# Optimization experiments

Measured on AMD Instinct MI355X. Metric: run time of the kernel, lower is better.

Reference implementation:

```python
import jax, jax.numpy as jnp
import numpy as np
import math

B, T, D, DI, DFF, H = 4, 1024, 1024, 256, 4096, 16
S, N, E = 16, 256, 1024          # stat_num, token_num, exemplar_len
STAT_K, TOKEN_K = 8, 16
NEG = -1e6


def setup_inputs() -> dict:
    key = jax.random.key(0)
    ks = jax.random.split(key, 32)
    r = lambda i, shape: jax.random.normal(ks[i], shape, jnp.float32)
    w = lambda i, shape: r(i, shape) * 0.02
    return dict(
        x=r(0, (B, T, D)),
        stat_enc=r(1, (B * S, N, D)),
        exemplar_enc=r(2, (B, E, D)),
        stat_feature=r(3, (B, S, D)),
        intent_embed=r(4, (B, 1, DI)),
        Wq1=w(5, (D, D)), Wk1=w(6, (D, D)), Wv1=w(7, (D, D)), Wo1=w(8, (D, D)),
        Wq_stat=w(9, (D + DI, D)), Wq_token=w(10, (D + DI, D)),
        Wk_stat=w(11, (D, D)), Wk_token=w(12, (D, D)),
        Wv_sel=w(13, (D, D)), Wo_sel=w(14, (D, D)),
        Wq2=w(15, (D + DI, D)), Wk2=w(16, (D, D)), Wv2=w(17, (D, D)), Wo2=w(18, (D, D)),
        Wg=w(19, (2 * D, 1)),
        W1=w(20, (D, DFF)), b1=jnp.zeros((DFF,), jnp.float32),
        W2=w(21, (DFF, D)), b2=jnp.zeros((D,), jnp.float32),
        g1=jnp.ones((D,), jnp.float32), be1=jnp.zeros((D,), jnp.float32),
        g2=jnp.ones((D,), jnp.float32), be2=jnp.zeros((D,), jnp.float32),
        g3=jnp.ones((D,), jnp.float32), be3=jnp.zeros((D,), jnp.float32),
        stat_valid_len=jax.random.randint(ks[22], (B,), 1, S + 1),
        example_valid_len=jax.random.randint(ks[23], (B,), 1, E + 1),
    )


def _ln(x, g, b):
    m = x.mean(-1, keepdims=True)
    v = ((x - m) ** 2).mean(-1, keepdims=True)
    return (x - m) / jnp.sqrt(v + 1e-5) * g + b


def _mha(q, k, v, valid, Wq, Wk, Wv, Wo):
    Bq, Tq, _ = q.shape
    Sk = k.shape[1]
    sp = lambda z: z.reshape(Bq, z.shape[1], H, -1).transpose(0, 2, 1, 3)  # B,H,L,dh
    qh, kh, vh = sp(q @ Wq), sp(k @ Wk), sp(v @ Wv)
    dh = qh.shape[-1]
    sc = jnp.einsum('bhtd,bhsd->bhts', qh, kh) / math.sqrt(dh)
    vl = valid[:, None, None, None] if valid.ndim == 1 else valid[:, None, :, None]
    sc = jnp.where(jnp.arange(Sk)[None, None, None, :] < vl, sc, NEG)
    w = jax.nn.softmax(sc, axis=-1)
    out = jnp.einsum('bhts,bhsd->bhtd', w, vh).transpose(0, 2, 1, 3).reshape(Bq, Tq, -1)
    return out @ Wo


def _scatter_topk(scores, k):
    # keep top-k per row, everything else -> NEG (matches torch topk+scatter)
    shp = scores.shape
    flat = scores.reshape(-1, shp[-1])
    vals, idx = jax.lax.top_k(flat, k)
    out = jnp.full_like(flat, NEG).at[jnp.arange(flat.shape[0])[:, None], idx].set(vals)
    return out.reshape(shp)


def reference(x, stat_enc, exemplar_enc, stat_feature, intent_embed,
              Wq1, Wk1, Wv1, Wo1,
              Wq_stat, Wq_token, Wk_stat, Wk_token, Wv_sel, Wo_sel,
              Wq2, Wk2, Wv2, Wo2, Wg,
              W1, b1, W2, b2,
              g1, be1, g2, be2, g3, be3,
              stat_valid_len, example_valid_len):
    # masked self-attention (training mode -> causal valid lens)
    dec_valid = jnp.broadcast_to(jnp.arange(1, T + 1)[None, :], (B, T))
    x2 = _mha(x, x, x, dec_valid, Wq1, Wk1, Wv1, Wo1)
    y = _ln(x + x2, g1, be1)
    yi = jnp.concatenate([y, jnp.broadcast_to(intent_embed, (B, T, DI))], axis=-1)

    # selective hierarchical top-k attention
    qs = yi @ Wq_stat                      # [B,T,D]
    qt = yi @ Wq_token                     # [B,T,D]
    ks = stat_feature @ Wk_stat            # [B,S,D]
    kt = (stat_enc @ Wk_token).reshape(B, S, N, D)
    vv = (stat_enc @ Wv_sel).reshape(B, S, N, D)
    scale = math.sqrt(D)
    ssc = jnp.einsum('btd,bsd->bts', qs, ks) / scale
    ssc = jnp.where(jnp.arange(S)[None, None, :] < stat_valid_len[:, None, None], ssc, NEG)
    sw = jax.nn.softmax(_scatter_topk(ssc, min(S - 1, STAT_K)), axis=-1)   # [B,T,S]
    tsc = jnp.einsum('btd,bsnd->btsn', qt, kt) / scale                      # [B,T,S,N]
    tw = jax.nn.softmax(_scatter_topk(tsc, min(N - 1, TOKEN_K)), axis=-1)
    comb = sw[..., None] * tw                                               # [B,T,S,N]
    y2s = jnp.einsum('btsn,bsnd->btd', comb, vv) @ Wo_sel

    # exemplar cross-attention
    y2e = _mha(yi, exemplar_enc, exemplar_enc, example_valid_len, Wq2, Wk2, Wv2, Wo2)

    gate = jax.nn.sigmoid(jnp.concatenate([y2s, y2e], axis=-1) @ Wg)
    y2 = gate * y2s + (1.0 - gate) * y2e
    z = _ln(y + 2.0 * y2, g2, be2)
    ffn = jax.nn.relu(z @ W1 + b1) @ W2 + b2
    return _ln(z + ffn, g3, be3)
```

## Files before the change

### kernel.cpp

```cpp
#include <hip/hip_runtime.h>

typedef unsigned short u16;
typedef short s16x8 __attribute__((ext_vector_type(8)));
typedef u16 u16x4 __attribute__((ext_vector_type(4)));
typedef float f32x4 __attribute__((ext_vector_type(4)));

#define T_N   1024
#define NEGV  -1e6f
#define MB    (1L << 20)

__device__ __forceinline__ u16 f2bf(float f) {
    unsigned u = __float_as_uint(f);
    u += 0x7fffu + ((u >> 16) & 1u);
    return (u16)(u >> 16);
}
__device__ __forceinline__ float bf2f(u16 h) {
    return __uint_as_float(((unsigned)h) << 16);
}
__device__ __forceinline__ f32x4 mfma16(s16x8 a, s16x8 b, f32x4 c) {
    return __builtin_amdgcn_mfma_f32_16x16x32_bf16(a, b, c, 0, 0, 0);
}
__device__ __forceinline__ void gll16(const u16* g, u16* l) {
    __builtin_amdgcn_global_load_lds((const __attribute__((address_space(1))) void*)g,
                                     (__attribute__((address_space(3))) void*)l, 16, 0, 0);
}

struct P6 { const float* s[6]; u16* d[6]; };

__global__ __launch_bounds__(256) void transpose_cast_batch(P6 pp, int K, int N) {
    const float* __restrict__ src = pp.s[blockIdx.z];
    u16* __restrict__ dst = pp.d[blockIdx.z];
    __shared__ float tile[32][33];
    int nb = blockIdx.x * 32, kb = blockIdx.y * 32;
    int tx = threadIdx.x & 31, ty = threadIdx.x >> 5;
    #pragma unroll
    for (int i = 0; i < 4; i++)
        tile[ty + 8*i][tx] = src[(long)(kb + ty + 8*i) * N + nb + tx];
    __syncthreads();
    #pragma unroll
    for (int i = 0; i < 4; i++)
        dst[(long)(nb + ty + 8*i) * K + kb + tx] = f2bf(tile[tx][ty + 8*i]);
}

__global__ __launch_bounds__(256) void cast_bf16_kernel(const float* __restrict__ src,
                                                        u16* __restrict__ dst, long n) {
    long i = ((long)blockIdx.x * 256 + threadIdx.x) * 4;
    if (i >= n) return;
    float4 v = *(const float4*)(src + i);
    u16x4 o = { f2bf(v.x), f2bf(v.y), f2bf(v.z), f2bf(v.w) };
    *(u16x4*)(dst + i) = o;
}

template<typename OutT, bool RELU, bool HAS_BIAS>
__global__ __launch_bounds__(256) void gemm_bt(
    const u16* __restrict__ A, const u16* __restrict__ Bt, OutT* __restrict__ C,
    const float* __restrict__ bias, int M, int N, int K,
    int lda, int ldb, int ldc,
    int batchDivA, long sA, long sB, long sC)
{
    A  += (long)(blockIdx.z / batchDivA) * sA;
    Bt += (long)blockIdx.z * sB;
    C  += (long)blockIdx.z * sC;
    __shared__ __align__(16) u16 As[4096];
    __shared__ __align__(16) u16 Bs[4096];
    const int tid = threadIdx.x;
    const int wave = tid >> 6, lane = tid & 63;
    const int quad = lane >> 4, l16 = lane & 15;
    const int wr = (wave >> 1) * 64, wc = (wave & 1) * 64;
    const long row0 = (long)blockIdx.y * 128, col0 = (long)blockIdx.x * 128;

    f32x4 acc[4][4] = {};

    const int l4r = lane >> 2;
    const int l4c = (lane & 3) * 8;
    const int ra = wave * 32 + l4r;
    const u16* Ap0 = A + (row0 + ra) * (long)lda + l4c;
    const u16* Ap1 = Ap0 + 16L * lda;
    const u16* Bp0 = Bt + (col0 + ra) * (long)ldb + l4c;
    const u16* Bp1 = Bp0 + 16L * ldb;
    u16* AsW0 = &As[(wave * 32) * 32];
    u16* AsW1 = &As[(wave * 32 + 16) * 32];
    u16* BsW0 = &Bs[(wave * 32) * 32];
    u16* BsW1 = &Bs[(wave * 32 + 16) * 32];
    const bool aok0 = (row0 + wave * 32) < M;
    const bool aok1 = (row0 + wave * 32 + 16) < M;

    for (int k0 = 0; k0 < K; k0 += 32) {
        __syncthreads();
        if (aok0) gll16(Ap0 + k0, AsW0);
        if (aok1) gll16(Ap1 + k0, AsW1);
        gll16(Bp0 + k0, BsW0);
        gll16(Bp1 + k0, BsW1);
        __syncthreads();
        s16x8 af[4], bfr[4];
        #pragma unroll
        for (int i = 0; i < 4; i++)
            af[i]  = *(const s16x8*)&As[(wr + i*16 + l16) * 32 + quad*8];
        #pragma unroll
        for (int j = 0; j < 4; j++)
            bfr[j] = *(const s16x8*)&Bs[(wc + j*16 + l16) * 32 + quad*8];
        #pragma unroll
        for (int i = 0; i < 4; i++)
            #pragma unroll
            for (int j = 0; j < 4; j++)
                acc[i][j] = mfma16(af[i], bfr[j], acc[i][j]);
    }

    #pragma unroll
    for (int i = 0; i < 4; i++) {
        long row = row0 + wr + i*16 + quad*4;
        #pragma unroll
        for (int j = 0; j < 4; j++) {
            long col = col0 + wc + j*16 + l16;
            float bv = 0.f;
            if constexpr (HAS_BIAS) bv = bias[col];
            #pragma unroll
            for (int r = 0; r < 4; r++) {
                if (row + r < M) {
                    float v = acc[i][j][r] + bv;
                    if constexpr (RELU) v = fmaxf(v, 0.f);
                    if constexpr (sizeof(OutT) == 2) C[(row + r) * (long)ldc + col] = f2bf(v);
                    else                             C[(row + r) * (long)ldc + col] = v;
                }
            }
        }
    }
}

template<typename OutT, bool RELU, bool HAS_BIAS>
__global__ __launch_bounds__(512, 2) void gemm_bt256(
    const u16* __restrict__ A, const u16* __restrict__ Bt, OutT* __restrict__ C,
    const float* __restrict__ bias, int M, int N, int K,
    int lda, int ldb, int ldc,
    int batchDivA, long sA, long sB, long sC)
{
    int bx = blockIdx.x, by = blockIdx.y;
    {
        const int nwg = gridDim.x * gridDim.y;
        if ((nwg & 7) == 0) {
            const int flat = by * gridDim.x + bx;
            const int nf = (flat & 7) * (nwg >> 3) + (flat >> 3);
            bx = nf % gridDim.x;
            by = nf / gridDim.x;
        }
    }
    A  += (long)(blockIdx.z / batchDivA) * sA;
    Bt += (long)blockIdx.z * sB;
    C  += (long)blockIdx.z * sC;
    __shared__ __align__(16) u16 As[4][8192];
    __shared__ __align__(16) u16 Bs[4][8192];
    const int tid = threadIdx.x;
    const int wave = tid >> 6, lane = tid & 63;
    const int quad = lane >> 4, l16 = lane & 15;
    const int wm = wave >> 2, wn = wave & 3;
    const long row0 = (long)by * 256, col0 = (long)bx * 256;

    const int srow = tid >> 2;
    const int scol = ((tid & 3) ^ ((srow >> 1) & 3)) * 8;
    const u16* Ag = A  + (row0 + srow) * (long)lda + scol;
    const u16* Bg = Bt + (col0 + srow) * (long)ldb + scol;
    const int ldsoff = wave * 512;

    f32x4 acc[8][4] = {};
    const int NT = K >> 5;

    auto stageA = [&](int kt, int buf) {
        gll16(Ag + (long)kt * 32,            &As[buf][ldsoff]);
        gll16(Ag + (long)kt * 32 + 128L*lda, &As[buf][4096 + ldsoff]);
    };
    auto stageB = [&](int kt, int buf) {
        gll16(Bg + (long)kt * 32,            &Bs[buf][ldsoff]);
        gll16(Bg + (long)kt * 32 + 128L*ldb, &Bs[buf][4096 + ldsoff]);
    };

    stageA(0, 0); stageB(0, 0);
    stageA(1, 1); stageB(1, 1);
    stageA(2, 2); stageB(2, 2);
    asm volatile("s_waitcnt vmcnt(8)" ::: "memory");
    __builtin_amdgcn_s_barrier();
    __builtin_amdgcn_sched_barrier(0);

    const int arow = wm * 128 + l16;
    const int brow = wn * 64  + l16;
    const int kq   = (quad ^ ((l16 >> 1) & 3)) * 8;

    for (int kt = 0; kt < NT; ++kt) {
        const int b  = kt & 3;
        const int sb = (kt + 3) & 3;
        const bool st = (kt + 3) < NT;
        const u16* Ab = As[b];
        const u16* Bb = Bs[b];

        s16x8 bfr[4], af[8];
        #pragma unroll
        for (int j = 0; j < 4; ++j)
            bfr[j] = *(const s16x8*)&Bb[(brow + j*16) * 32 + kq];
        #pragma unroll
        for (int i = 0; i < 8; ++i)
            af[i] = *(const s16x8*)&Ab[(arow + i*16) * 32 + kq];

        if (st) { stageA(kt + 3, sb); stageB(kt + 3, sb); }

        #pragma unroll
        for (int i = 0; i < 8; ++i)
            #pragma unroll
            for (int j = 0; j < 4; ++j)
                acc[i][j] = mfma16(af[i], bfr[j], acc[i][j]);

        const int rem = NT - 2 - kt;
        if (rem >= 2)      asm volatile("s_waitcnt vmcnt(8)" ::: "memory");
        else if (rem == 1) asm volatile("s_waitcnt vmcnt(4)" ::: "memory");
        else if (rem == 0) asm volatile("s_waitcnt vmcnt(0)" ::: "memory");
        __builtin_amdgcn_s_barrier();
        __builtin_amdgcn_sched_barrier(0);
    }

    #pragma unroll
    for (int i = 0; i < 8; ++i) {
        const long row = row0 + wm*128 + i*16 + quad*4;
        #pragma unroll
        for (int j = 0; j < 4; ++j) {
            const long col = col0 + wn*64 + j*16 + l16;
            float bv = 0.f;
            if constexpr (HAS_BIAS) bv = bias[col];
            #pragma unroll
            for (int r = 0; r < 4; ++r) {
                float v = acc[i][j][r] + bv;
                if constexpr (RELU) v = fmaxf(v, 0.f);
                if constexpr (sizeof(OutT) == 2) C[(row + r) * (long)ldc + col] = f2bf(v);
                else                             C[(row + r) * (long)ldc + col] = v;
            }
        }
    }
}

template<bool CAUSAL>
__global__ __launch_bounds__(256) void flash_attn_kernel(
    const u16* __restrict__ Q, const u16* __restrict__ Kg, const u16* __restrict__ Vg,
    const int* __restrict__ valid_len, u16* __restrict__ O,
    int qld, int kld, int vld)
{
    const int h = blockIdx.y, b = blockIdx.z;
    const int qt0 = blockIdx.x * 64;
    const int tid = threadIdx.x;
    const int wave = tid >> 6, lane = tid & 63;
    const int quad = lane >> 4, l16 = lane & 15;

    __shared__ __align__(16) u16 Qs[64][72];
    __shared__ __align__(16) u16 Ks[64][72];
    __shared__ __align__(16) u16 Vt[64][72];
    __shared__ __align__(16) u16 Ps[4][16][72];

    const int sr = tid >> 2, scc = (tid & 3) * 16;
    {
        const u16* qp = Q + ((long)b * T_N + qt0 + sr) * qld + h * 64 + scc;
        *(s16x8*)&Qs[sr][scc]     = *(const s16x8*)qp;
        *(s16x8*)&Qs[sr][scc + 8] = *(const s16x8*)(qp + 8);
    }
    float m_i[4] = {-1e30f, -1e30f, -1e30f, -1e30f};
    float l_i[4] = {0.f, 0.f, 0.f, 0.f};
    f32x4 o_acc[4] = {};

    int vl = 0, kend;
    if (CAUSAL) kend = qt0 + 64;
    else { vl = valid_len[b]; kend = (vl + 63) & ~63; }

    for (int kv0 = 0; kv0 < kend; kv0 += 64) {
        __syncthreads();
        {
            const u16* kp = Kg + ((long)b * T_N + kv0 + sr) * kld + h * 64 + scc;
            *(s16x8*)&Ks[sr][scc]     = *(const s16x8*)kp;
            *(s16x8*)&Ks[sr][scc + 8] = *(const s16x8*)(kp + 8);
            const u16* vp = Vg + ((long)b * T_N + kv0 + sr) * vld + h * 64 + scc;
            s16x8 v0 = *(const s16x8*)vp;
            s16x8 v1 = *(const s16x8*)(vp + 8);
            #pragma unroll
            for (int j = 0; j < 8; j++) {
                Vt[scc + j][sr]     = (u16)v0[j];
                Vt[scc + 8 + j][sr] = (u16)v1[j];
            }
        }
        __syncthreads();
        f32x4 sc[4] = {};
        #pragma unroll
        for (int kk = 0; kk < 64; kk += 32) {
            s16x8 aq = *(const s16x8*)&Qs[wave*16 + l16][kk + quad*8];
            #pragma unroll
            for (int j = 0; j < 4; j++) {
                s16x8 bk = *(const s16x8*)&Ks[j*16 + l16][kk + quad*8];
                sc[j] = mfma16(aq, bk, sc[j]);
            }
        }
        const int qrow = qt0 + wave*16 + quad*4;
        #pragma unroll
        for (int j = 0; j < 4; j++) {
            int kcol = kv0 + j*16 + l16;
            #pragma unroll
            for (int r = 0; r < 4; r++) {
                float s = sc[j][r] * 0.125f;
                bool ok = CAUSAL ? (kcol <= qrow + r) : (kcol < vl);
                sc[j][r] = ok ? s : -1e30f;
            }
        }
        float alpha[4];
        #pragma unroll
        for (int r = 0; r < 4; r++) {
            float mx = fmaxf(fmaxf(sc[0][r], sc[1][r]), fmaxf(sc[2][r], sc[3][r]));
            #pragma unroll
            for (int d = 1; d < 16; d <<= 1) mx = fmaxf(mx, __shfl_xor(mx, d, 64));
            float mn = fmaxf(m_i[r], mx);
            alpha[r] = __expf(m_i[r] - mn);
            m_i[r] = mn;
        }
        float rsum[4] = {0.f, 0.f, 0.f, 0.f};
        #pragma unroll
        for (int j = 0; j < 4; j++)
            #pragma unroll
            for (int r = 0; r < 4; r++) {
                float pv = __expf(sc[j][r] - m_i[r]);
                sc[j][r] = pv;
                rsum[r] += pv;
            }
        #pragma unroll
        for (int r = 0; r < 4; r++) {
            #pragma unroll
            for (int d = 1; d < 16; d <<= 1) rsum[r] += __shfl_xor(rsum[r], d, 64);
            l_i[r] = l_i[r] * alpha[r] + rsum[r];
        }
        #pragma unroll
        for (int j = 0; j < 4; j++)
            #pragma unroll
            for (int r = 0; r < 4; r++)
                Ps[wave][quad*4 + r][j*16 + l16] = f2bf(sc[j][r]);
        #pragma unroll
        for (int j2 = 0; j2 < 4; j2++)
            #pragma unroll
            for (int r = 0; r < 4; r++)
                o_acc[j2][r] *= alpha[r];
        __syncthreads();
        #pragma unroll
        for (int kk = 0; kk < 64; kk += 32) {
            s16x8 ap = *(const s16x8*)&Ps[wave][l16][kk + quad*8];
            #pragma unroll
            for (int j2 = 0; j2 < 4; j2++) {
                s16x8 bv = *(const s16x8*)&Vt[j2*16 + l16][kk + quad*8];
                o_acc[j2] = mfma16(ap, bv, o_acc[j2]);
            }
        }
    }
    #pragma unroll
    for (int j2 = 0; j2 < 4; j2++) {
        #pragma unroll
        for (int r = 0; r < 4; r++) {
            float v = o_acc[j2][r] / l_i[r];
            long row = (long)b * T_N + qt0 + wave*16 + quad*4 + r;
            O[row * 1024 + h*64 + j2*16 + l16] = f2bf(v);
        }
    }
}

__global__ __launch_bounds__(256) void ssc_kernel(
    const u16* __restrict__ qs, const u16* __restrict__ ks,
    const int* __restrict__ svl, float* __restrict__ ssc, int qld)
{
    const int t = blockIdx.x, b = blockIdx.y;
    const int wave = threadIdx.x >> 6, lane = threadIdx.x & 63;
    const u16* qrow = qs + ((long)b * T_N + t) * qld + lane * 16;
    const int vl = svl[b];
    for (int s = wave; s < 16; s += 4) {
        const u16* krow = ks + ((long)b * 16 + s) * 1024 + lane * 16;
        float acc = 0.f;
        #pragma unroll
        for (int seg = 0; seg < 2; seg++) {
            s16x8 qv = *(const s16x8*)(qrow + seg*8);
            s16x8 kv = *(const s16x8*)(krow + seg*8);
            #pragma unroll
            for (int j = 0; j < 8; j++) acc += bf2f((u16)qv[j]) * bf2f((u16)kv[j]);
        }
        #pragma unroll
        for (int d = 1; d < 64; d <<= 1) acc += __shfl_xor(acc, d, 64);
        if (lane == 0)
            ssc[((long)b * T_N + t) * 16 + s] = (s < vl) ? acc * (1.f/32.f) : NEGV;
    }
}

__global__ __launch_bounds__(256) void select_combine_kernel(
    const float* __restrict__ ssc, const float* __restrict__ tsc,
    const u16* __restrict__ vv, u16* __restrict__ out, int t0, int vld)
{
    const int tl = blockIdx.x, b = blockIdx.y;
    const int tg = t0 + tl;
    const int tid = threadIdx.x;
    const int wave = tid >> 6, lane = tid & 63;
    __shared__ float coeff[128];
    __shared__ long  rowoff[128];
    __shared__ int   sel_s[8];
    __shared__ float sel_w[8];

    if (wave == 0) {
        float cur = (lane < 16) ? ssc[((long)b * T_N + tg) * 16 + lane] : -3e38f;
        float mx0 = 0.f, ssum = 0.f, myv = -3e38f;
        int myi = 0;
        #pragma unroll
        for (int it = 0; it < 8; it++) {
            float mv = cur; int mi = lane;
            #pragma unroll
            for (int d = 1; d < 64; d <<= 1) {
                float ov = __shfl_xor(mv, d, 64);
                int   oi = __shfl_xor(mi, d, 64);
                if (ov > mv || (ov == mv && oi < mi)) { mv = ov; mi = oi; }
            }
            if (it == 0) mx0 = mv;
            ssum += __expf(mv - mx0);
            if (lane == it) { myv = mv; myi = mi; }
            if (lane == mi) cur = -3e38f;
        }
        if (lane < 8) { sel_s[lane] = myi; sel_w[lane] = __expf(myv - mx0) / ssum; }
    }
    __syncthreads();

    for (int slot = wave; slot < 8; slot += 4) {
        int s = sel_s[slot];
        float sw = sel_w[slot];
        const float* trow = tsc + (((long)b * 16 + s) * 512 + tl) * 256;
        float4 lv4 = *(const float4*)(trow + lane * 4);
        float loc[4] = { lv4.x, lv4.y, lv4.z, lv4.w };
        float mx0 = 0.f, tsum = 0.f, myv = -3e38f;
        int myi = 0;
        for (int it = 0; it < 16; it++) {
            float mv = -3e38f; int mi = 0;
            #pragma unroll
            for (int u = 0; u < 4; u++)
                if (loc[u] > mv) { mv = loc[u]; mi = lane*4 + u; }
            #pragma unroll
            for (int d = 1; d < 64; d <<= 1) {
                float ov = __shfl_xor(mv, d, 64);
                int   oi = __shfl_xor(mi, d, 64);
                if (ov > mv || (ov == mv && oi < mi)) { mv = ov; mi = oi; }
            }
            if (it == 0) mx0 = mv * (1.f/32.f);
            tsum += __expf(mv * (1.f/32.f) - mx0);
            if (lane == it) { myv = mv; myi = mi; }
            if ((mi >> 2) == lane) {
                int u = mi & 3;
                if (u == 0) loc[0] = -3e38f;
                else if (u == 1) loc[1] = -3e38f;
                else if (u == 2) loc[2] = -3e38f;
                else loc[3] = -3e38f;
            }
        }
        if (lane < 16) {
            coeff[slot * 16 + lane]  = sw * __expf(myv * (1.f/32.f) - mx0) / tsum;
            rowoff[slot * 16 + lane] = (long)((b * 16 + s) * 256 + myi) * vld;
        }
    }
    __syncthreads();

    const int d0 = tid * 4;
    float a0 = 0.f, a1 = 0.f, a2 = 0.f, a3 = 0.f;
    for (int r = 0; r < 128; r++) {
        float c = coeff[r];
        const u16* vp = vv + rowoff[r] + d0;
        u16x4 v4 = *(const u16x4*)vp;
        a0 += c * bf2f(v4[0]);
        a1 += c * bf2f(v4[1]);
        a2 += c * bf2f(v4[2]);
        a3 += c * bf2f(v4[3]);
    }
    u16x4 o4 = { f2bf(a0), f2bf(a1), f2bf(a2), f2bf(a3) };
    *(u16x4*)(out + ((long)b * T_N + tg) * 1024 + d0) = o4;
}

__device__ __forceinline__ float block_sum(float v, float* red) {
    #pragma unroll
    for (int d = 1; d < 64; d <<= 1) v += __shfl_xor(v, d, 64);
    __syncthreads();
    if ((threadIdx.x & 63) == 0) red[threadIdx.x >> 6] = v;
    __syncthreads();
    return red[0] + red[1] + red[2] + red[3];
}

__global__ __launch_bounds__(256) void ln1_kernel(
    const float* __restrict__ x, const float* __restrict__ x2,
    const float* __restrict__ intent, const float* __restrict__ g, const float* __restrict__ be,
    u16* __restrict__ yi)
{
    __shared__ float red[4];
    const long row = blockIdx.x;
    const int tid = threadIdx.x;
    const long base = row * 1024 + tid * 4;
    float4 xv = *(const float4*)(x + base);
    float4 dv = *(const float4*)(x2 + base);
    float h0 = xv.x + dv.x, h1 = xv.y + dv.y, h2 = xv.z + dv.z, h3 = xv.w + dv.w;
    float s1 = block_sum(h0 + h1 + h2 + h3, red);
    float s2 = block_sum(h0*h0 + h1*h1 + h2*h2 + h3*h3, red);
    float mean = s1 * (1.f/1024.f);
    float var = s2 * (1.f/1024.f) - mean * mean;
    float inv = rsqrtf(var + 1e-5f);
    const int c = tid * 4;
    float4 gv = *(const float4*)(g + c);
    float4 bv = *(const float4*)(be + c);
    float o0 = (h0 - mean) * inv * gv.x + bv.x;
    float o1 = (h1 - mean) * inv * gv.y + bv.y;
    float o2 = (h2 - mean) * inv * gv.z + bv.z;
    float o3 = (h3 - mean) * inv * gv.w + bv.w;
    u16x4 ob = { f2bf(o0), f2bf(o1), f2bf(o2), f2bf(o3) };
    *(u16x4*)(yi + row * 1280 + c) = ob;
    const int b = (int)(row >> 10);
    yi[row * 1280 + 1024 + tid] = f2bf(intent[b * 256 + tid]);
}

__global__ __launch_bounds__(256) void gate_ln2_kernel(
    const u16* __restrict__ yi, const float* __restrict__ y2s, const float* __restrict__ y2e,
    const float* __restrict__ Wg, const float* __restrict__ g, const float* __restrict__ be,
    float* __restrict__ z, u16* __restrict__ zbf)
{
    __shared__ float red[4];
    const long row = blockIdx.x;
    const int tid = threadIdx.x;
    const long base = row * 1024 + tid * 4;
    const int c = tid * 4;
    float4 sv = *(const float4*)(y2s + base);
    float4 ev = *(const float4*)(y2e + base);
    float4 w1 = *(const float4*)(Wg + c);
    float4 w2 = *(const float4*)(Wg + 1024 + c);
    float dot = sv.x*w1.x + sv.y*w1.y + sv.z*w1.z + sv.w*w1.w
              + ev.x*w2.x + ev.y*w2.y + ev.z*w2.z + ev.w*w2.w;
    float tot = block_sum(dot, red);
    float gate = 1.f / (1.f + __expf(-tot));
    u16x4 yv4 = *(const u16x4*)(yi + row * 1280 + c);
    float h0 = bf2f(yv4[0]) + 2.f * (gate * sv.x + (1.f - gate) * ev.x);
    float h1 = bf2f(yv4[1]) + 2.f * (gate * sv.y + (1.f - gate) * ev.y);
    float h2 = bf2f(yv4[2]) + 2.f * (gate * sv.z + (1.f - gate) * ev.z);
    float h3 = bf2f(yv4[3]) + 2.f * (gate * sv.w + (1.f - gate) * ev.w);
    float s1 = block_sum(h0 + h1 + h2 + h3, red);
    float s2 = block_sum(h0*h0 + h1*h1 + h2*h2 + h3*h3, red);
    float mean = s1 * (1.f/1024.f);
    float var = s2 * (1.f/1024.f) - mean * mean;
    float inv = rsqrtf(var + 1e-5f);
    float4 gv = *(const float4*)(g + c);
    float4 bv = *(const float4*)(be + c);
    float o0 = (h0 - mean) * inv * gv.x + bv.x;
    float o1 = (h1 - mean) * inv * gv.y + bv.y;
    float o2 = (h2 - mean) * inv * gv.z + bv.z;
    float o3 = (h3 - mean) * inv * gv.w + bv.w;
    *(float4*)(z + base) = make_float4(o0, o1, o2, o3);
    u16x4 ob = { f2bf(o0), f2bf(o1), f2bf(o2), f2bf(o3) };
    *(u16x4*)(zbf + row * 1024 + c) = ob;
}

__global__ __launch_bounds__(256) void ln3_kernel(
    const float* __restrict__ z, const float* __restrict__ p0, const float* __restrict__ p1,
    const float* __restrict__ b2,
    const float* __restrict__ g, const float* __restrict__ be, float* __restrict__ out)
{
    __shared__ float red[4];
    const long row = blockIdx.x;
    const int tid = threadIdx.x;
    const long base = row * 1024 + tid * 4;
    const int c = tid * 4;
    float4 zv = *(const float4*)(z + base);
    float4 f0 = *(const float4*)(p0 + base);
    float4 f1 = *(const float4*)(p1 + base);
    float4 bb = *(const float4*)(b2 + c);
    float h0 = zv.x + f0.x + f1.x + bb.x;
    float h1 = zv.y + f0.y + f1.y + bb.y;
    float h2 = zv.z + f0.z + f1.z + bb.z;
    float h3 = zv.w + f0.w + f1.w + bb.w;
    float s1 = block_sum(h0 + h1 + h2 + h3, red);
    float s2 = block_sum(h0*h0 + h1*h1 + h2*h2 + h3*h3, red);
    float mean = s1 * (1.f/1024.f);
    float var = s2 * (1.f/1024.f) - mean * mean;
    float inv = rsqrtf(var + 1e-5f);
    float4 gv = *(const float4*)(g + c);
    float4 bv = *(const float4*)(be + c);
    float o0 = (h0 - mean) * inv * gv.x + bv.x;
    float o1 = (h1 - mean) * inv * gv.y + bv.y;
    float o2 = (h2 - mean) * inv * gv.z + bv.z;
    float o3 = (h3 - mean) * inv * gv.w + bv.w;
    *(float4*)(out + base) = make_float4(o0, o1, o2, o3);
}

extern "C" void kernel_launch(void* const* d_in, const int* in_sizes, int n_in,
                              void* d_out, int out_size, void* d_ws, size_t ws_size,
                              hipStream_t stream)
{
    (void)in_sizes; (void)n_in; (void)out_size; (void)ws_size;
    const float* x      = (const float*)d_in[0];
    const float* stat_e = (const float*)d_in[1];
    const float* exem   = (const float*)d_in[2];
    const float* sfeat  = (const float*)d_in[3];
    const float* intent = (const float*)d_in[4];
    const float* Wg  = (const float*)d_in[19];
    const float* b1  = (const float*)d_in[21];
    const float* b2  = (const float*)d_in[23];
    const float* g1  = (const float*)d_in[24]; const float* be1 = (const float*)d_in[25];
    const float* g2  = (const float*)d_in[26]; const float* be2 = (const float*)d_in[27];
    const float* g3  = (const float*)d_in[28]; const float* be3 = (const float*)d_in[29];
    const int* svl = (const int*)d_in[30];
    const int* evl = (const int*)d_in[31];
    float* outp = (float*)d_out;

    char* base = (char*)d_ws;
    u16*  bufA  = (u16*)(base + 0*MB);
    u16*  qkv1  = (u16*)(base + 8*MB);
    float* x2a  = (float*)(base + 8*MB);
    u16*  kv2   = (u16*)(base + 8*MB);
    u16*  w1t   = (u16*)(base + 8*MB);
    u16*  w2t   = (u16*)(base + 16*MB);
    u16*  yibf  = (u16*)(base + 32*MB);
    u16*  buf3  = (u16*)(base + 42*MB);
    u16*  zbf   = (u16*)(base + 42*MB);
    u16*  sebf  = (u16*)(base + 66*MB);
    float* tsch = (float*)(base + 66*MB);
    u16*  hid   = (u16*)(base + 66*MB);
    u16*  ktvv  = (u16*)(base + 98*MB);
    float* y2sf = (float*)(base + 98*MB);
    float* p0f  = (float*)(base + 98*MB);
    u16*  exbf  = (u16*)(base + 114*MB);
    float* y2ef = (float*)(base + 122*MB);
    float* zf   = (float*)(base + 138*MB);
    u16*  sfbf  = (u16*)(base + 162*MB);
    u16*  ksbf  = (u16*)(base + 162*MB + 256*1024);
    float* sscf = (float*)(base + 162*MB + 512*1024);
    char* wpool = base + 163*MB;

    dim3 blk(256);
    dim3 blk512(512);
    auto cast = [&](const float* s, u16* d, long n) {
        cast_bf16_kernel<<<dim3((unsigned)((n/4 + 255) / 256)), blk, 0, stream>>>(s, d, n);
    };
    auto g_n = [&](const u16* A, const u16* Bt, u16* C, int M, int N, int K,
                   int lda, int ldb, int ldc) {
        gemm_bt<u16,false,false><<<dim3(N/128, (M+127)/128, 1), blk, 0, stream>>>(
            A, Bt, C, nullptr, M, N, K, lda, ldb, ldc, 1, 0, 0, 0);
    };
    auto g_f = [&](const u16* A, const u16* Bt, float* C, int M, int N, int K,
                   int lda, int ldb, int ldc) {
        gemm_bt<float,false,false><<<dim3(N/128, (M+127)/128, 1), blk, 0, stream>>>(
            A, Bt, C, nullptr, M, N, K, lda, ldb, ldc, 1, 0, 0, 0);
    };
    auto g256_n = [&](const u16* A, const u16* Bt, u16* C, int M, int N, int K,
                      int lda, int ldb, int ldc) {
        gemm_bt256<u16,false,false><<<dim3(N/256, M/256, 1), blk512, 0, stream>>>(
            A, Bt, C, nullptr, M, N, K, lda, ldb, ldc, 1, 0, 0, 0);
    };

    u16* wqkv1t = (u16*)wpool;
    u16* wo1t   = (u16*)(wpool) + 3L*1024*1024;
    {
        P6 pp{};
        pp.s[0]=(const float*)d_in[5]; pp.d[0]=wqkv1t;
        pp.s[1]=(const float*)d_in[6]; pp.d[1]=wqkv1t + 1L*1024*1024;
        pp.s[2]=(const float*)d_in[7]; pp.d[2]=wqkv1t + 2L*1024*1024;
        pp.s[3]=(const float*)d_in[8]; pp.d[3]=wo1t;
        transpose_cast_batch<<<dim3(32, 32, 4), blk, 0, stream>>>(pp, 1024, 1024);
    }
    cast(x, bufA, 4096L*1024);
    g256_n(bufA, wqkv1t, qkv1, 4096, 3072, 1024, 1024, 1024, 3072);
    flash_attn_kernel<true><<<dim3(16, 16, 4), blk, 0, stream>>>(
        qkv1, qkv1 + 1024, qkv1 + 2048, nullptr, bufA, 3072, 3072, 3072);
    g_f(bufA, wo1t, x2a, 4096, 1024, 1024, 1024, 1024, 1024);
    ln1_kernel<<<dim3(4096), blk, 0, stream>>>(x, x2a, intent, g1, be1, yibf);

    u16* wq3t = (u16*)wpool;
    {
        P6 pp{};
        pp.s[0]=(const float*)d_in[9];  pp.d[0]=wq3t;
        pp.s[1]=(const float*)d_in[10]; pp.d[1]=wq3t + 1L*1024*1280;
        pp.s[2]=(const float*)d_in[15]; pp.d[2]=wq3t + 2L*1024*1280;
        transpose_cast_batch<<<dim3(32, 40, 3), blk, 0, stream>>>(pp, 1280, 1024);
    }
    g256_n(yibf, wq3t, buf3, 4096, 3072, 1280, 1280, 1280, 3072);
    u16* wkst = (u16*)wpool;
    u16* wkv  = (u16*)(wpool) + 1L*1024*1024;
    {
        P6 pp{};
        pp.s[0]=(const float*)d_in[11]; pp.d[0]=wkst;
        pp.s[1]=(const float*)d_in[12]; pp.d[1]=wkv;
        pp.s[2]=(const float*)d_in[13]; pp.d[2]=wkv + 1L*1024*1024;
        transpose_cast_batch<<<dim3(32, 32, 3), blk, 0, stream>>>(pp, 1024, 1024);
    }
    cast(sfeat, sfbf, 64L*1024);
    cast(stat_e, sebf, 16384L*1024);
    g_n(sfbf, wkst, ksbf, 64, 1024, 1024, 1024, 1024, 1024);
    g256_n(sebf, wkv, ktvv, 16384, 2048, 1024, 1024, 1024, 2048);
    ssc_kernel<<<dim3(1024, 4), blk, 0, stream>>>(buf3, ksbf, svl, sscf, 3072);
    for (int hh = 0; hh < 2; hh++) {
        long t0 = hh * 512;
        gemm_bt<float,false,false><<<dim3(2, 4, 64), blk, 0, stream>>>(
            buf3 + 1024 + t0*3072, ktvv, tsch, nullptr, 512, 256, 1024,
            3072, 2048, 256, 16, (long)T_N*3072, 256L*2048, 512L*256);
        select_combine_kernel<<<dim3(512, 4), blk, 0, stream>>>(
            sscf, tsch, ktvv + 1024, bufA, (int)t0, 2048);
    }
    u16* wost = (u16*)wpool;
    u16* wkv2 = (u16*)(wpool) + 1L*1024*1024;
    u16* wo2t = (u16*)(wpool) + 3L*1024*1024;
    {
        P6 pp{};
        pp.s[0]=(const float*)d_in[14]; pp.d[0]=wost;
        pp.s[1]=(const float*)d_in[16]; pp.d[1]=wkv2;
        pp.s[2]=(const float*)d_in[17]; pp.d[2]=wkv2 + 1L*1024*1024;
        pp.s[3]=(const float*)d_in[18]; pp.d[3]=wo2t;
        transpose_cast_batch<<<dim3(32, 32, 4), blk, 0, stream>>>(pp, 1024, 1024);
    }
    g_f(bufA, wost, y2sf, 4096, 1024, 1024, 1024, 1024, 1024);

    cast(exem, exbf, 4096L*1024);
    g_n(exbf, wkv2, kv2, 4096, 2048, 1024, 1024, 1024, 2048);
    flash_attn_kernel<false><<<dim3(16, 16, 4), blk, 0, stream>>>(
        buf3 + 2048, kv2, kv2 + 1024, evl, bufA, 3072, 2048, 2048);
    g_f(bufA, wo2t, y2ef, 4096, 1024, 1024, 1024, 1024, 1024);

    gate_ln2_kernel<<<dim3(4096), blk, 0, stream>>>(yibf, y2sf, y2ef, Wg, g2, be2, zf, zbf);

    {
        P6 pp{}; pp.s[0] = (const float*)d_in[20]; pp.d[0] = w1t;
        transpose_cast_batch<<<dim3(128, 32, 1), blk, 0, stream>>>(pp, 1024, 4096);
    }
    {
        P6 pp{}; pp.s[0] = (const float*)d_in[22]; pp.d[0] = w2t;
        transpose_cast_batch<<<dim3(32, 128, 1), blk, 0, stream>>>(pp, 4096, 1024);
    }
    gemm_bt256<u16,true,true><<<dim3(16, 16, 1), blk512, 0, stream>>>(
        zbf, w1t, hid, b1, 4096, 4096, 1024, 1024, 1024, 4096, 1, 0, 0, 0);
    gemm_bt<float,false,false><<<dim3(8, 32, 2), blk, 0, stream>>>(
        hid, w2t, p0f, nullptr, 4096, 1024, 2048, 4096, 4096, 1024,
        1, 2048, 2048, 4096L*1024);

    ln3_kernel<<<dim3(4096), blk, 0, stream>>>(zf, p0f, p0f + 4096L*1024, b2, g3, be3, outp);
}
```

Measured before the change: 1.005 ms.

## Double-buffer K/V tiles with register prefetch and swizzled LDS in flash attention

Restructures the flash attention loop so the next K/V tile is loaded from global memory into registers while the current tile is being computed, then stored into a second LDS buffer. This cuts the per-iteration barriers from two to one. Q fragments are held in registers rather than LDS, LDS arrays are unpadded with an XOR swizzle to avoid bank conflicts, and MFMA sections get raised wave priority. The kernel also gets an occupancy hint of 4 blocks per CU. Register pressure increases and the swizzled indexing adds address arithmetic.

```diff
diff --git a/kernel.cpp b/kernel.cpp
--- a/kernel.cpp
+++ b/kernel.cpp
@@ -23,6 +23,12 @@
 __device__ __forceinline__ void gll16(const u16* g, u16* l) {
     __builtin_amdgcn_global_load_lds((const __attribute__((address_space(1))) void*)g,
                                      (__attribute__((address_space(3))) void*)l, 16, 0, 0);
+}
+__device__ __forceinline__ int swzf(int row) {
+    return ((row >> 1) & 3) | ((row & 1) << 2);
+}
+__device__ __forceinline__ int swzc(int col, int row) {
+    return (((col >> 3) ^ swzf(row)) << 3) | (col & 7);
 }
 
 struct P6 { const float* s[6]; u16* d[6]; };
@@ -235,7 +241,7 @@
 }
 
 template<bool CAUSAL>
-__global__ __launch_bounds__(256) void flash_attn_kernel(
+__global__ __launch_bounds__(256, 4) void flash_attn_kernel(
     const u16* __restrict__ Q, const u16* __restrict__ Kg, const u16* __restrict__ Vg,
     const int* __restrict__ valid_len, u16* __restrict__ O,
     int qld, int kld, int vld)
@@ -246,17 +252,30 @@
     const int wave = tid >> 6, lane = tid & 63;
     const int quad = lane >> 4, l16 = lane & 15;
 
-    __shared__ __align__(16) u16 Qs[64][72];
-    __shared__ __align__(16) u16 Ks[64][72];
-    __shared__ __align__(16) u16 Vt[64][72];
-    __shared__ __align__(16) u16 Ps[4][16][72];
-
-    const int sr = tid >> 2, scc = (tid & 3) * 16;
-    {
-        const u16* qp = Q + ((long)b * T_N + qt0 + sr) * qld + h * 64 + scc;
-        *(s16x8*)&Qs[sr][scc]     = *(const s16x8*)qp;
-        *(s16x8*)&Qs[sr][scc + 8] = *(const s16x8*)(qp + 8);
-    }
+    __shared__ __align__(16) u16 Ks[2][64][64];
+    __shared__ __align__(16) u16 Vt[2][64][64];
+    __shared__ __align__(16) u16 Ps[4][16][64];
+
+    s16x8 aq[2];
+    {
+        const u16* qp = Q + ((long)b * T_N + qt0 + wave*16 + l16) * qld + h * 64 + quad * 8;
+        aq[0] = *(const s16x8*)qp;
+        aq[1] = *(const s16x8*)(qp + 32);
+    }
+
+    const int ksr = tid >> 2;
+    const int ks2 = (tid & 3) * 2;
+    const int vsr = tid & 63;
+    const int vd0 = (tid >> 6) * 16;
+
+    const u16* kp = Kg + ((long)b * T_N + ksr) * (long)kld + h * 64 + ks2 * 8;
+    const u16* vp = Vg + ((long)b * T_N + vsr) * (long)vld + h * 64 + vd0;
+    const long kstep = 64L * kld, vstep = 64L * vld;
+
+    const int fl  = swzf(l16);
+    const int kc0 = ((quad ^ fl) & 7) * 8;
+    const int kc1 = (((quad + 4) ^ fl) & 7) * 8;
+
     float m_i[4] = {-1e30f, -1e30f, -1e30f, -1e30f};
     float l_i[4] = {0.f, 0.f, 0.f, 0.f};
     f32x4 o_acc[4] = {};
@@ -264,39 +283,51 @@
     int vl = 0, kend;
     if (CAUSAL) kend = qt0 + 64;
     else { vl = valid_len[b]; kend = (vl + 63) & ~63; }
-
-    for (int kv0 = 0; kv0 < kend; kv0 += 64) {
-        __syncthreads();
-        {
-            const u16* kp = Kg + ((long)b * T_N + kv0 + sr) * kld + h * 64 + scc;
-            *(s16x8*)&Ks[sr][scc]     = *(const s16x8*)kp;
-            *(s16x8*)&Ks[sr][scc + 8] = *(const s16x8*)(kp + 8);
-            const u16* vp = Vg + ((long)b * T_N + kv0 + sr) * vld + h * 64 + scc;
-            s16x8 v0 = *(const s16x8*)vp;
-            s16x8 v1 = *(const s16x8*)(vp + 8);
-            #pragma unroll
-            for (int j = 0; j < 8; j++) {
-                Vt[scc + j][sr]     = (u16)v0[j];
-                Vt[scc + 8 + j][sr] = (u16)v1[j];
-            }
-        }
-        __syncthreads();
+    const int nt = kend >> 6;
+
+    s16x8 krA, krB, vrA, vrB;
+    krA = *(const s16x8*)kp;       krB = *(const s16x8*)(kp + 8);
+    vrA = *(const s16x8*)vp;       vrB = *(const s16x8*)(vp + 8);
+    kp += kstep; vp += vstep;
+    {
+        *(s16x8*)&Ks[0][ksr][swzc(ks2*8,     ksr)] = krA;
+        *(s16x8*)&Ks[0][ksr][swzc(ks2*8 + 8, ksr)] = krB;
+        #pragma unroll
+        for (int j = 0; j < 8; ++j) {
+            Vt[0][vd0 + j    ][swzc(vsr, vd0 + j    )] = (u16)vrA[j];
+            Vt[0][vd0 + 8 + j][swzc(vsr, vd0 + 8 + j)] = (u16)vrB[j];
+        }
+    }
+    __syncthreads();
+
+    for (int t = 0; t < nt; ++t) {
+        const int cur = t & 1;
+        const bool more = (t + 1) < nt;
+        if (more) {
+            krA = *(const s16x8*)kp;  krB = *(const s16x8*)(kp + 8);
+            vrA = *(const s16x8*)vp;  vrB = *(const s16x8*)(vp + 8);
+            kp += kstep; vp += vstep;
+        }
         f32x4 sc[4] = {};
-        #pragma unroll
-        for (int kk = 0; kk < 64; kk += 32) {
-            s16x8 aq = *(const s16x8*)&Qs[wave*16 + l16][kk + quad*8];
-            #pragma unroll
-            for (int j = 0; j < 4; j++) {
-                s16x8 bk = *(const s16x8*)&Ks[j*16 + l16][kk + quad*8];
-                sc[j] = mfma16(aq, bk, sc[j]);
-            }
-        }
+        __builtin_amdgcn_s_setprio(1);
+        #pragma unroll
+        for (int j = 0; j < 4; ++j) {
+            s16x8 bk0 = *(const s16x8*)&Ks[cur][j*16 + l16][kc0];
+            sc[j] = mfma16(aq[0], bk0, sc[j]);
+        }
+        #pragma unroll
+        for (int j = 0; j < 4; ++j) {
+            s16x8 bk1 = *(const s16x8*)&Ks[cur][j*16 + l16][kc1];
+            sc[j] = mfma16(aq[1], bk1, sc[j]);
+        }
+        __builtin_amdgcn_s_setprio(0);
+        const int kv0 = t * 64;
         const int qrow = qt0 + wave*16 + quad*4;
         #pragma unroll
-        for (int j = 0; j < 4; j++) {
+        for (int j = 0; j < 4; ++j) {
             int kcol = kv0 + j*16 + l16;
             #pragma unroll
-            for (int r = 0; r < 4; r++) {
+            for (int r = 0; r < 4; ++r) {
                 float s = sc[j][r] * 0.125f;
                 bool ok = CAUSAL ? (kcol <= qrow + r) : (kcol < vl);
                 sc[j][r] = ok ? s : -1e30f;
@@ -304,7 +335,7 @@
         }
         float alpha[4];
         #pragma unroll
-        for (int r = 0; r < 4; r++) {
+        for (int r = 0; r < 4; ++r) {
             float mx = fmaxf(fmaxf(sc[0][r], sc[1][r]), fmaxf(sc[2][r], sc[3][r]));
             #pragma unroll
             for (int d = 1; d < 16; d <<= 1) mx = fmaxf(mx, __shfl_xor(mx, d, 64));
@@ -314,44 +345,62 @@
         }
         float rsum[4] = {0.f, 0.f, 0.f, 0.f};
         #pragma unroll
-        for (int j = 0; j < 4; j++)
-            #pragma unroll
-            for (int r = 0; r < 4; r++) {
+        for (int j = 0; j < 4; ++j)
+            #pragma unroll
+            for (int r = 0; r < 4; ++r) {
                 float pv = __expf(sc[j][r] - m_i[r]);
                 sc[j][r] = pv;
                 rsum[r] += pv;
             }
         #pragma unroll
-        for (int r = 0; r < 4; r++) {
+        for (int r = 0; r < 4; ++r) {
             #pragma unroll
             for (int d = 1; d < 16; d <<= 1) rsum[r] += __shfl_xor(rsum[r], d, 64);
             l_i[r] = l_i[r] * alpha[r] + rsum[r];
         }
         #pragma unroll
-        for (int j = 0; j < 4; j++)
-            #pragma unroll
-            for (int r = 0; r < 4; r++)
-                Ps[wave][quad*4 + r][j*16 + l16] = f2bf(sc[j][r]);
-        #pragma unroll
-        for (int j2 = 0; j2 < 4; j2++)
-            #pragma unroll
-            for (int r = 0; r < 4; r++)
+        for (int j = 0; j < 4; ++j)
+            #pragma unroll
+            for (int r = 0; r < 4; ++r)
+                Ps[wave][quad*4 + r][swzc(j*16 + l16, quad*4 + r)] = f2bf(sc[j][r]);
+        #pragma unroll
+        for (int j2 = 0; j2 < 4; ++j2)
+            #pragma unroll
+            for (int r = 0; r < 4; ++r)
                 o_acc[j2][r] *= alpha[r];
+        __builtin_amdgcn_s_setprio(1);
+        {
+            s16x8 ap0 = *(const s16x8*)&Ps[wave][l16][kc0];
+            #pragma unroll
+            for (int j2 = 0; j2 < 4; ++j2) {
+                s16x8 bv = *(const s16x8*)&Vt[cur][j2*16 + l16][kc0];
+                o_acc[j2] = mfma16(ap0, bv, o_acc[j2]);
+            }
+            s16x8 ap1 = *(const s16x8*)&Ps[wave][l16][kc1];
+            #pragma unroll
+            for (int j2 = 0; j2 < 4; ++j2) {
+                s16x8 bv = *(const s16x8*)&Vt[cur][j2*16 + l16][kc1];
+                o_acc[j2] = mfma16(ap1, bv, o_acc[j2]);
+            }
+        }
+        __builtin_amdgcn_s_setprio(0);
+        if (more) {
+            const int nb = cur ^ 1;
+            *(s16x8*)&Ks[nb][ksr][swzc(ks2*8,     ksr)] = krA;
+            *(s16x8*)&Ks[nb][ksr][swzc(ks2*8 + 8, ksr)] = krB;
+            #pragma unroll
+            for (int j = 0; j < 8; ++j) {
+                Vt[nb][vd0 + j    ][swzc(vsr, vd0 + j    )] = (u16)vrA[j];
+                Vt[nb][vd0 + 8 + j][swzc(vsr, vd0 + 8 + j)] = (u16)vrB[j];
+            }
+        }
         __syncthreads();
-        #pragma unroll
-        for (int kk = 0; kk < 64; kk += 32) {
-            s16x8 ap = *(const s16x8*)&Ps[wave][l16][kk + quad*8];
-            #pragma unroll
-            for (int j2 = 0; j2 < 4; j2++) {
-                s16x8 bv = *(const s16x8*)&Vt[j2*16 + l16][kk + quad*8];
-                o_acc[j2] = mfma16(ap, bv, o_acc[j2]);
-            }
-        }
-    }
+    }
+
     #pragma unroll
-    for (int j2 = 0; j2 < 4; j2++) {
-        #pragma unroll
-        for (int r = 0; r < 4; r++) {
+    for (int j2 = 0; j2 < 4; ++j2) {
+        #pragma unroll
+        for (int r = 0; r < 4; ++r) {
             float v = o_acc[j2][r] / l_i[r];
             long row = (long)b * T_N + qt0 + wave*16 + quad*4 + r;
             O[row * 1024 + h*64 + j2*16 + l16] = f2bf(v);
```

Result: no change. 988.0 us (-1.7%).
